# Optimization experiments

Measured on AMD Instinct MI355X. Metric: run time of the kernel, lower is better.

Reference implementation:

```python
import jax, jax.numpy as jnp
import numpy as np

DIM, NH, WS, SR, CTS = 256, 8, 8, 4, 2
HD = DIM // NH
SCALE = HD ** -0.5

def _linear(x, w, b=None):
    y = x @ w.T
    return y + b if b is not None else y

def _ln(x, g, b, eps=1e-5):
    m = jnp.mean(x, -1, keepdims=True)
    v = jnp.mean((x - m) ** 2, -1, keepdims=True)
    return (x - m) / jnp.sqrt(v + eps) * g + b

def _mlp(x, w1, b1, w2, b2):
    return _linear(jax.nn.gelu(_linear(x, w1, b1), approximate=False), w2, b2)

def _pos_emb_rank3(seq_len, w1, b1, w2):
    # PosEmbMLPSwinv1D with rank=3: coords on cube_root(seq) grid, normalized
    s = int(round(seq_len ** (1.0 / 3.0)))
    c = (jnp.arange(s, dtype=jnp.float32) - s // 2) / (s // 2)
    grid = jnp.stack(jnp.meshgrid(c, c, c, indexing='ij'))      # (3,s,s,s)
    tbl = grid.reshape(3, -1).T                                 # (s^3,3)
    return _linear(jax.nn.relu(_linear(tbl, w1, b1)), w2)[None]  # (1,s^3,dim)

def _rel_bias_3d(ws, w1, b1, w2, n_global):
    # PosEmbMLPSwinv3D: CPB-MLP bias over 3D relative coords, 16*sigmoid, zero-pad for carrier tokens
    r = jnp.arange(-(ws - 1), ws, dtype=jnp.float32)
    tbl = jnp.stack(jnp.meshgrid(r, r, r, indexing='ij'), axis=-1) / (ws - 1)
    tbl = tbl * 8.0
    tbl = jnp.sign(tbl) * jnp.log2(jnp.abs(tbl) + 1.0) / np.log2(8.0)
    table = _linear(jax.nn.relu(_linear(tbl.reshape(-1, 3), w1, b1)), w2)  # ((2ws-1)^3, NH)
    coords = jnp.stack(jnp.meshgrid(jnp.arange(ws), jnp.arange(ws), jnp.arange(ws), indexing='ij'))
    cf = coords.reshape(3, -1)
    rel = (cf[:, :, None] - cf[:, None, :]).transpose(1, 2, 0) + (ws - 1)  # (P,P,3)
    idx = rel[..., 0] * (2 * ws - 1) ** 2 + rel[..., 1] * (2 * ws - 1) + rel[..., 2]
    P = ws ** 3
    bias = table[idx.reshape(-1)].reshape(P, P, NH).transpose(2, 0, 1)
    bias = 16.0 * jax.nn.sigmoid(bias)
    return jnp.pad(bias, ((0, 0), (n_global, 0), (n_global, 0)))[None]  # (1,NH,P+g,P+g)

def _win_attn(x, qkv_w, qkv_b, proj_w, proj_b, bias):
    B, N, C = x.shape
    qkv = _linear(x, qkv_w, qkv_b).reshape(B, N, 3, NH, HD).transpose(2, 0, 3, 1, 4)
    q, k, v = qkv[0], qkv[1], qkv[2]
    attn = jax.nn.softmax(jnp.einsum('bhnd,bhmd->bhnm', q, k) * SCALE + bias, axis=-1)
    out = jnp.einsum('bhnm,bhmd->bhnd', attn, v).transpose(0, 2, 1, 3).reshape(B, N, C)
    return _linear(out, proj_w, proj_b)

def _ct_dewindow(ct, W, H, D, ws):
    bs, _, N = ct.shape
    c = ct.reshape(bs, W // ws, H // ws, D // ws, ws, ws, ws, N)
    c = c.transpose(0, 7, 1, 3, 5, 2, 4, 6).reshape(bs, N, W * H * D)
    return c.transpose(0, 2, 1)

def _ct_window(ct, W, H, D, ws):
    bs, _, N = ct.shape
    c = ct.reshape(bs, H // ws, ws, W // ws, ws, D // ws, ws, N)
    return c.transpose(0, 1, 3, 5, 2, 4, 6, 7)

def setup_inputs() -> dict:
    key = jax.random.key(0)
    ks = jax.random.split(key, 48)
    B0 = 1
    nw = SR ** 3
    def w(k, *s):
        return jax.random.normal(k, s, jnp.float32) * 0.02
    def b(k, *s):
        return jax.random.normal(k, s, jnp.float32) * 0.01
    d4 = 4 * DIM
    return {
        'x': jax.random.normal(ks[0], (B0 * nw, WS ** 3, DIM), jnp.float32),
        'ct': jax.random.normal(ks[1], (B0, (CTS * SR) ** 3, DIM), jnp.float32),
        'pe_w1': w(ks[2], 512, 3), 'pe_b1': b(ks[3], 512), 'pe_w2': w(ks[4], DIM, 512),
        'hpe_w1': w(ks[5], 512, 3), 'hpe_b1': b(ks[6], 512), 'hpe_w2': w(ks[7], DIM, 512),
        'hat_n1_g': jnp.ones((DIM,), jnp.float32), 'hat_n1_b': jnp.zeros((DIM,), jnp.float32),
        'hat_qkv_w': w(ks[8], 3 * DIM, DIM), 'hat_qkv_b': b(ks[9], 3 * DIM),
        'hat_proj_w': w(ks[10], DIM, DIM), 'hat_proj_b': b(ks[11], DIM),
        'hat_cpb_w1': w(ks[12], 512, 3), 'hat_cpb_b1': b(ks[13], 512), 'hat_cpb_w2': w(ks[14], NH, 512),
        'hat_n2_g': jnp.ones((DIM,), jnp.float32), 'hat_n2_b': jnp.zeros((DIM,), jnp.float32),
        'hat_fc1_w': w(ks[15], d4, DIM), 'hat_fc1_b': b(ks[16], d4),
        'hat_fc2_w': w(ks[17], DIM, d4), 'hat_fc2_b': b(ks[18], DIM),
        'n1_g': jnp.ones((DIM,), jnp.float32), 'n1_b': jnp.zeros((DIM,), jnp.float32),
        'qkv_w': w(ks[19], 3 * DIM, DIM), 'qkv_b': b(ks[20], 3 * DIM),
        'proj_w': w(ks[21], DIM, DIM), 'proj_b': b(ks[22], DIM),
        'cpb_w1': w(ks[23], 512, 3), 'cpb_b1': b(ks[24], 512), 'cpb_w2': w(ks[25], NH, 512),
        'n2_g': jnp.ones((DIM,), jnp.float32), 'n2_b': jnp.zeros((DIM,), jnp.float32),
        'fc1_w': w(ks[26], d4, DIM), 'fc1_b': b(ks[27], d4),
        'fc2_w': w(ks[28], DIM, d4), 'fc2_b': b(ks[29], DIM),
    }

def reference(x, ct, pe_w1, pe_b1, pe_w2, hpe_w1, hpe_b1, hpe_w2,
              hat_n1_g, hat_n1_b, hat_qkv_w, hat_qkv_b, hat_proj_w, hat_proj_b,
              hat_cpb_w1, hat_cpb_b1, hat_cpb_w2, hat_n2_g, hat_n2_b,
              hat_fc1_w, hat_fc1_b, hat_fc2_w, hat_fc2_b,
              n1_g, n1_b, qkv_w, qkv_b, proj_w, proj_b,
              cpb_w1, cpb_b1, cpb_w2, n2_g, n2_b, fc1_w, fc1_b, fc2_w, fc2_b):
    Bg, Ng, Hg = ct.shape
    G = CTS * SR  # carrier-token global cube side
    x = x + _pos_emb_rank3(x.shape[1], pe_w1, pe_b1, pe_w2)
    # carrier-token global attention (hierarchical path)
    ct = _ct_dewindow(ct, G, G, G, CTS)
    ct = ct + _pos_emb_rank3(ct.shape[1], hpe_w1, hpe_b1, hpe_w2)
    hat_bias = _rel_bias_3d(G, hat_cpb_w1, hat_cpb_b1, hat_cpb_w2, 0)
    ct = ct + _win_attn(_ln(ct, hat_n1_g, hat_n1_b), hat_qkv_w, hat_qkv_b, hat_proj_w, hat_proj_b, hat_bias)
    ct = ct + _mlp(_ln(ct, hat_n2_g, hat_n2_b), hat_fc1_w, hat_fc1_b, hat_fc2_w, hat_fc2_b)
    ct_w = _ct_window(ct, G, G, G, CTS).reshape(x.shape[0], -1, Hg)
    # windowed attention over [carrier tokens ; window tokens]
    x = jnp.concatenate([ct_w, x], axis=1)
    bias = _rel_bias_3d(WS, cpb_w1, cpb_b1, cpb_w2, CTS ** 3)
    x = x + _win_attn(_ln(x, n1_g, n1_b), qkv_w, qkv_b, proj_w, proj_b, bias)
    x = x + _mlp(_ln(x, n2_g, n2_b), fc1_w, fc1_b, fc2_w, fc2_b)
    split = x.shape[1] - WS ** 3
    ctr, x = x[:, :split], x[:, split:]
    return x, ctr.reshape(Bg, Ng, Hg)
```

## Files before the change

### kernel.cpp

```cpp
#include <hip/hip_runtime.h>
#include <hip/hip_bf16.h>
#include <math.h>

typedef __hip_bfloat16 bf16;

#define SCALE_QK 0.17677669529663687f

__device__ __forceinline__ float b2f(bf16 v){ return __bfloat162float(v); }
__device__ __forceinline__ bf16  f2b(float v){ return __float2bfloat16(v); }
__device__ __forceinline__ short bfs(float x){ bf16 b = f2b(x); short s; __builtin_memcpy(&s, &b, 2); return s; }

struct __align__(16) bf16x8 { bf16 v[8]; };
struct __align__(8)  bf16x4 { bf16 v[4]; };

typedef __attribute__((ext_vector_type(8))) short sh8;
typedef __attribute__((ext_vector_type(4))) short sh4;
typedef __attribute__((ext_vector_type(4))) float f4;

#if defined(__has_builtin)
#if __has_builtin(__builtin_amdgcn_mfma_f32_16x16x16bf16_1k)
#define HAS_MFMA16 1
#else
#define HAS_MFMA16 0
#endif
#else
#define HAS_MFMA16 0
#endif

#if defined(__has_builtin)
#if __has_builtin(__builtin_amdgcn_exp2f)
#define EXP2(x) __builtin_amdgcn_exp2f(x)
#else
#define EXP2(x) exp2f(x)
#endif
#else
#define EXP2(x) exp2f(x)
#endif

__device__ __forceinline__ void gl16(const bf16* g, short* l) {
    __builtin_amdgcn_global_load_lds((const __attribute__((address_space(1))) void*)g,
                                     (__attribute__((address_space(3))) void*)l, 16, 0, 0);
}

__global__ __launch_bounds__(256) void wcvt10_k(const float* s0, const float* s1, const float* s2, const float* s3,
                                                const float* s4, const float* s5, const float* s6, const float* s7,
                                                const float* s8, const float* s9,
                                                bf16* d0, bf16* d1, bf16* d2, bf16* d3, bf16* d4,
                                                bf16* d5, bf16* d6, bf16* d7, bf16* d8, bf16* d9) {
    const int sizes[10] = {196608, 65536, 262144, 262144, 196608, 65536, 262144, 262144, 131072, 131072};
    int which = blockIdx.y;
    const float* s; bf16* d;
    switch (which) {
        case 0: s = s0; d = d0; break;  case 1: s = s1; d = d1; break;
        case 2: s = s2; d = d2; break;  case 3: s = s3; d = d3; break;
        case 4: s = s4; d = d4; break;  case 5: s = s5; d = d5; break;
        case 6: s = s6; d = d6; break;  case 7: s = s7; d = d7; break;
        case 8: s = s8; d = d8; break;  default: s = s9; d = d9; break;
    }
    int i = blockIdx.x * 256 + threadIdx.x;
    if (i < sizes[which]) d[i] = f2b(s[i]);
}

__global__ __launch_bounds__(256) void hidbuild_k(const float* __restrict__ w1a, const float* __restrict__ b1a,
                                                  const float* __restrict__ w1b, const float* __restrict__ b1b,
                                                  bf16* __restrict__ hidA, bf16* __restrict__ hidB) {
    const float* w1 = blockIdx.y ? w1b : w1a;
    const float* b1 = blockIdx.y ? b1b : b1a;
    bf16* hid       = blockIdx.y ? hidB : hidA;
    int t = blockIdx.x, tid = threadIdx.x;
    int i = t >> 6, j = (t >> 3) & 7, k = t & 7;
    float c0 = (i - 4) * 0.25f, c1 = (j - 4) * 0.25f, c2 = (k - 4) * 0.25f;
    #pragma unroll
    for (int rep = 0; rep < 2; rep++) {
        int jj = tid + rep * 256;
        float h = c0 * w1[jj*3+0] + c1 * w1[jj*3+1] + c2 * w1[jj*3+2] + b1[jj];
        hid[(size_t)t * 512 + jj] = f2b(fmaxf(h, 0.f));
    }
}

__device__ __forceinline__ float cpb_coord(int idx) {
    float v = (idx - 7) * (8.0f / 7.0f);
    return copysignf(log2f(fabsf(v) + 1.0f) * (1.0f / 3.0f), v);
}
__global__ __launch_bounds__(512) void cpbtab_k(const float* __restrict__ w1a, const float* __restrict__ b1a,
                                                const float* __restrict__ w2a, float* __restrict__ taba,
                                                const float* __restrict__ w1b, const float* __restrict__ b1b,
                                                const float* __restrict__ w2b, float* __restrict__ tabb) {
    const float* w1 = blockIdx.y ? w1b : w1a;
    const float* b1 = blockIdx.y ? b1b : b1a;
    const float* w2 = blockIdx.y ? w2b : w2a;
    float* tab      = blockIdx.y ? tabb : taba;
    int t = blockIdx.x, tid = threadIdx.x;
    __shared__ float hid[512];
    int i = t / 225, r = t - i * 225, j = r / 15, k = r - j * 15;
    float x0 = cpb_coord(i), x1 = cpb_coord(j), x2 = cpb_coord(k);
    float h = x0 * w1[tid*3+0] + x1 * w1[tid*3+1] + x2 * w1[tid*3+2] + b1[tid];
    hid[tid] = fmaxf(h, 0.f);
    __syncthreads();
    int h8 = tid >> 6, lane = tid & 63;
    float p = 0.f;
    for (int jj = lane; jj < 512; jj += 64) p += hid[jj] * w2[h8*512 + jj];
    for (int off = 32; off; off >>= 1) p += __shfl_down(p, off);
    if (lane == 0) tab[t * 8 + h8] = p;
}

__global__ __launch_bounds__(256) void biasbuild_k(const float* __restrict__ taba, float* __restrict__ biasQa,
                                                   const float* __restrict__ tabb, float* __restrict__ biasQb) {
    const float* tab = blockIdx.y ? tabb : taba;
    float* biasQ     = blockIdx.y ? biasQb : biasQa;
    int idx = blockIdx.x * 256 + threadIdx.x;
    int h = idx >> 18, rem = idx & 262143;
    int q = rem >> 9, k = rem & 511;
    int qx = q >> 6, qy = (q >> 3) & 7, qz = q & 7;
    int kx = k >> 6, ky = (k >> 3) & 7, kz = k & 7;
    int tidx = ((qx - kx + 7) * 15 + (qy - ky + 7)) * 15 + (qz - kz + 7);
    float v = tab[tidx * 8 + h];
    float b = 16.f / (1.f + __expf(-v));
    biasQ[idx] = (b - 24.0f) * 1.4426950408889634f;
}

__global__ __launch_bounds__(256) void ct0ln_k(const float* __restrict__ ct_in,
                                               const float* __restrict__ hpe,
                                               const float* __restrict__ g,
                                               const float* __restrict__ b,
                                               float* __restrict__ ct0,
                                               bf16* __restrict__ lnout) {
    int u = blockIdx.x, c = threadIdx.x;
    int a = u >> 7, cc = (u >> 5) & 3, e = (u >> 4) & 1, bb = (u >> 2) & 3, d = (u >> 1) & 1, f = u & 1;
    int t = a * 128 + bb * 32 + cc * 8 + d * 4 + e * 2 + f;
    float x = ct_in[(size_t)t * 256 + c] + hpe[(size_t)u * 256 + c];
    ct0[(size_t)u * 256 + c] = x;
    float s = x, s2 = x * x;
    for (int off = 32; off; off >>= 1) { s += __shfl_down(s, off); s2 += __shfl_down(s2, off); }
    __shared__ float red[8];
    int wid = c >> 6, lane = c & 63;
    if (lane == 0) { red[wid] = s; red[wid + 4] = s2; }
    __syncthreads();
    if (c == 0) { red[0] = red[0] + red[1] + red[2] + red[3]; red[4] = red[4] + red[5] + red[6] + red[7]; }
    __syncthreads();
    float mean = red[0] * (1.f / 256.f);
    float var  = fmaxf(red[4] * (1.f / 256.f) - mean * mean, 0.f);
    float rstd = rsqrtf(var + 1e-5f);
    lnout[(size_t)u * 256 + c] = f2b((x - mean) * rstd * g[c] + b[c]);
}

__global__ __launch_bounds__(256) void ln_k(const float* __restrict__ in,
                                            const float* __restrict__ g,
                                            const float* __restrict__ b,
                                            bf16* __restrict__ out) {
    int row = blockIdx.x, c = threadIdx.x;
    float x = in[(size_t)row * 256 + c];
    float s = x, s2 = x * x;
    for (int off = 32; off; off >>= 1) { s += __shfl_down(s, off); s2 += __shfl_down(s2, off); }
    __shared__ float red[8];
    int wid = c >> 6, lane = c & 63;
    if (lane == 0) { red[wid] = s; red[wid + 4] = s2; }
    __syncthreads();
    if (c == 0) { red[0] = red[0] + red[1] + red[2] + red[3]; red[4] = red[4] + red[5] + red[6] + red[7]; }
    __syncthreads();
    float mean = red[0] * (1.f / 256.f);
    float var  = fmaxf(red[4] * (1.f / 256.f) - mean * mean, 0.f);
    float rstd = rsqrtf(var + 1e-5f);
    out[(size_t)row * 256 + c] = f2b((x - mean) * rstd * g[c] + b[c]);
}

template <int MODE>
__global__ __launch_bounds__(256) void gemm_k(const bf16* __restrict__ A,
                                              const bf16* __restrict__ W,
                                              const float* __restrict__ bias,
                                              int M, int N, int K,
                                              float* __restrict__ res,
                                              bf16* __restrict__ outb) {
    __shared__ short As[128 * 32];
    __shared__ short Ws[128 * 32];
    int m0 = blockIdx.y * 128, n0 = blockIdx.x * 128;
    int tid = threadIdx.x;
    int lane = tid & 63, wave = tid >> 6;
    int quad = lane >> 4, m16 = lane & 15;
    int wm = (wave & 1) * 64, wn = (wave >> 1) * 64;
    int arow = tid >> 2, acol = (tid & 3) * 8;

    const bf16* Ab = A + (size_t)(m0 + arow) * K + acol;
    const bf16* A2 = Ab + (size_t)64 * K;
    const bf16* Wb = W + (size_t)(n0 + arow) * K + acol;
    const bf16* W2 = Wb + (size_t)64 * K;
    short* dA0 = &As[tid * 8];
    short* dA1 = &As[2048 + tid * 8];
    short* dW0 = &Ws[tid * 8];
    short* dW1 = &Ws[2048 + tid * 8];

    f4 acc[4][4];
    #pragma unroll
    for (int i = 0; i < 4; i++)
        #pragma unroll
        for (int j = 0; j < 4; j++) acc[i][j] = (f4){0.f, 0.f, 0.f, 0.f};

    for (int k0 = 0; k0 < K; k0 += 32) {
        __syncthreads();
        gl16(Ab + k0, dA0);
        gl16(A2 + k0, dA1);
        gl16(Wb + k0, dW0);
        gl16(W2 + k0, dW1);
        __syncthreads();
        sh8 af[4], bf[4];
        #pragma unroll
        for (int mi = 0; mi < 4; mi++)
            af[mi] = *reinterpret_cast<const sh8*>(&As[(wm + mi * 16 + m16) * 32 + quad * 8]);
        #pragma unroll
        for (int ni = 0; ni < 4; ni++)
            bf[ni] = *reinterpret_cast<const sh8*>(&Ws[(wn + ni * 16 + m16) * 32 + quad * 8]);
        #pragma unroll
        for (int mi = 0; mi < 4; mi++)
            #pragma unroll
            for (int ni = 0; ni < 4; ni++)
                acc[mi][ni] = __builtin_amdgcn_mfma_f32_16x16x32_bf16(af[mi], bf[ni], acc[mi][ni], 0, 0, 0);
    }
    (void)M;

    #pragma unroll
    for (int mi = 0; mi < 4; mi++) {
        #pragma unroll
        for (int r = 0; r < 4; r++) {
            int gm = m0 + wm + mi * 16 + quad * 4 + r;
            #pragma unroll
            for (int ni = 0; ni < 4; ni++) {
                int gn = n0 + wn + ni * 16 + m16;
                float v = acc[mi][ni][r];
                if constexpr (MODE != 3) v += bias[gn];
                if constexpr (MODE == 2)      res[(size_t)gm * N + gn] += v;
                else if constexpr (MODE == 3) res[(size_t)gm * N + gn] = v;
                else if constexpr (MODE == 1) outb[(size_t)gm * N + gn] = f2b(0.5f * v * (1.0f + erff(v * 0.70710678118654752f)));
                else                          outb[(size_t)gm * N + gn] = f2b(v);
            }
        }
    }
}

__global__ __launch_bounds__(512) void gemmln_k(const bf16* __restrict__ A,
                                                const bf16* __restrict__ W,
                                                const float* __restrict__ bias,
                                                float* __restrict__ xcat,
                                                const float* __restrict__ g,
                                                const float* __restrict__ b,
                                                bf16* __restrict__ outb) {
    __shared__ short As[128 * 32];
    __shared__ short Ws[256 * 32];
    __shared__ float redS[128 * 4];
    __shared__ float redQ[128 * 4];
    __shared__ float stat[128 * 2];
    int m0 = blockIdx.x * 128;
    int tid = threadIdx.x;
    int lane = tid & 63, wave = tid >> 6;
    int quad = lane >> 4, m16 = lane & 15;
    int wm = (wave >> 2) * 64, wn = (wave & 3) * 64;
    int arow = tid >> 2, acol = (tid & 3) * 8;

    const bf16* Ab = A + (size_t)(m0 + (arow & 127)) * 256 + acol;
    const bf16* Wb = W + (size_t)arow * 256 + acol;
    const bf16* W2 = Wb + (size_t)128 * 256;
    short* dA0 = &As[(tid & 511) * 8 < 4096 ? tid * 8 : 0];

    f4 acc[4][4];
    #pragma unroll
    for (int i = 0; i < 4; i++)
        #pragma unroll
        for (int j = 0; j < 4; j++) acc[i][j] = (f4){0.f, 0.f, 0.f, 0.f};

    for (int k0 = 0; k0 < 256; k0 += 32) {
        __syncthreads();
        gl16(Ab + k0, &As[tid * 8]);
        gl16(Wb + k0, &Ws[tid * 8]);
        gl16(W2 + k0, &Ws[4096 + tid * 8]);
        __syncthreads();
        sh8 af[4], bf[4];
        #pragma unroll
        for (int mi = 0; mi < 4; mi++)
            af[mi] = *reinterpret_cast<const sh8*>(&As[(wm + mi * 16 + m16) * 32 + quad * 8]);
        #pragma unroll
        for (int ni = 0; ni < 4; ni++)
            bf[ni] = *reinterpret_cast<const sh8*>(&Ws[(wn + ni * 16 + m16) * 32 + quad * 8]);
        #pragma unroll
        for (int mi = 0; mi < 4; mi++)
            #pragma unroll
            for (int ni = 0; ni < 4; ni++)
                acc[mi][ni] = __builtin_amdgcn_mfma_f32_16x16x32_bf16(af[mi], bf[ni], acc[mi][ni], 0, 0, 0);
    }
    (void)dA0;

    #pragma unroll
    for (int mi = 0; mi < 4; mi++) {
        #pragma unroll
        for (int r = 0; r < 4; r++) {
            int lr = wm + mi * 16 + quad * 4 + r;
            int gm = m0 + lr;
            float ps = 0.f, pq = 0.f;
            #pragma unroll
            for (int ni = 0; ni < 4; ni++) {
                int gc = wn + ni * 16 + m16;
                float v = acc[mi][ni][r] + bias[gc] + xcat[(size_t)gm * 256 + gc];
                acc[mi][ni][r] = v;
                ps += v; pq += v * v;
            }
            ps += __shfl_xor(ps, 1); pq += __shfl_xor(pq, 1);
            ps += __shfl_xor(ps, 2); pq += __shfl_xor(pq, 2);
            ps += __shfl_xor(ps, 4); pq += __shfl_xor(pq, 4);
            ps += __shfl_xor(ps, 8); pq += __shfl_xor(pq, 8);
            if (m16 == 0) { redS[lr * 4 + (wave & 3)] = ps; redQ[lr * 4 + (wave & 3)] = pq; }
        }
    }
    __syncthreads();
    if (tid < 128) {
        float s = redS[tid * 4] + redS[tid * 4 + 1] + redS[tid * 4 + 2] + redS[tid * 4 + 3];
        float q = redQ[tid * 4] + redQ[tid * 4 + 1] + redQ[tid * 4 + 2] + redQ[tid * 4 + 3];
        float mean = s * (1.f / 256.f);
        float var  = fmaxf(q * (1.f / 256.f) - mean * mean, 0.f);
        stat[tid * 2]     = mean;
        stat[tid * 2 + 1] = rsqrtf(var + 1e-5f);
    }
    __syncthreads();
    #pragma unroll
    for (int mi = 0; mi < 4; mi++) {
        #pragma unroll
        for (int r = 0; r < 4; r++) {
            int lr = wm + mi * 16 + quad * 4 + r;
            int gm = m0 + lr;
            float mean = stat[lr * 2], rstd = stat[lr * 2 + 1];
            #pragma unroll
            for (int ni = 0; ni < 4; ni++) {
                int gc = wn + ni * 16 + m16;
                float v = acc[mi][ni][r];
                xcat[(size_t)gm * 256 + gc] = v;
                outb[(size_t)gm * 256 + gc] = f2b((v - mean) * rstd * g[gc] + b[gc]);
            }
        }
    }
}

__global__ __launch_bounds__(256) void gemmsplit_k(const bf16* __restrict__ A,
                                                   const bf16* __restrict__ W,
                                                   const float* __restrict__ bias,
                                                   int K,
                                                   const float* __restrict__ res,
                                                   float* __restrict__ out) {
    __shared__ short As[128 * 32];
    __shared__ short Ws[128 * 32];
    int m0 = blockIdx.y * 128, n0 = blockIdx.x * 128;
    int tid = threadIdx.x;
    int lane = tid & 63, wave = tid >> 6;
    int quad = lane >> 4, m16 = lane & 15;
    int wm = (wave & 1) * 64, wn = (wave >> 1) * 64;
    int arow = tid >> 2, acol = (tid & 3) * 8;

    const bf16* Ab = A + (size_t)(m0 + arow) * K + acol;
    const bf16* A2 = Ab + (size_t)64 * K;
    const bf16* Wb = W + (size_t)(n0 + arow) * K + acol;
    const bf16* W2 = Wb + (size_t)64 * K;

    f4 acc[4][4];
    #pragma unroll
    for (int i = 0; i < 4; i++)
        #pragma unroll
        for (int j = 0; j < 4; j++) acc[i][j] = (f4){0.f, 0.f, 0.f, 0.f};

    for (int k0 = 0; k0 < K; k0 += 32) {
        __syncthreads();
        gl16(Ab + k0, &As[tid * 8]);
        gl16(A2 + k0, &As[2048 + tid * 8]);
        gl16(Wb + k0, &Ws[tid * 8]);
        gl16(W2 + k0, &Ws[2048 + tid * 8]);
        __syncthreads();
        sh8 af[4], bf[4];
        #pragma unroll
        for (int mi = 0; mi < 4; mi++)
            af[mi] = *reinterpret_cast<const sh8*>(&As[(wm + mi * 16 + m16) * 32 + quad * 8]);
        #pragma unroll
        for (int ni = 0; ni < 4; ni++)
            bf[ni] = *reinterpret_cast<const sh8*>(&Ws[(wn + ni * 16 + m16) * 32 + quad * 8]);
        #pragma unroll
        for (int mi = 0; mi < 4; mi++)
            #pragma unroll
            for (int ni = 0; ni < 4; ni++)
                acc[mi][ni] = __builtin_amdgcn_mfma_f32_16x16x32_bf16(af[mi], bf[ni], acc[mi][ni], 0, 0, 0);
    }

    #pragma unroll
    for (int mi = 0; mi < 4; mi++) {
        #pragma unroll
        for (int r = 0; r < 4; r++) {
            int gm = m0 + wm + mi * 16 + quad * 4 + r;
            int w = gm / 520, p = gm - w * 520;
            size_t drow = (p >= 8) ? (size_t)(w * 512 + p - 8) : (size_t)(32768 + w * 8 + p);
            #pragma unroll
            for (int ni = 0; ni < 4; ni++) {
                int gn = n0 + wn + ni * 16 + m16;
                float v = acc[mi][ni][r] + bias[gn] + res[(size_t)gm * 256 + gn];
                out[drow * 256 + gn] = v;
            }
        }
    }
}

#define VSTR 548
#define SC2   0.25503575360579045f
#define CNB  (-34.62468098133512f)
#define NEGB (-1.0e30f)
__global__ __launch_bounds__(512) void flash_k(const bf16* __restrict__ qkv,
                                               const float* __restrict__ biasQ,
                                               bf16* __restrict__ out,
                                               int N, int glob) {
    int wh = blockIdx.x, w = wh >> 3, h = wh & 7;
    int qs = blockIdx.y;
    int tid = threadIdx.x;
    int lane = tid & 63, wave = tid >> 6;
    int quad = lane >> 4, qcol = lane & 15;
    const int NT32 = (N + 31) & ~31;

    __shared__ __align__(16) char smem[32 * VSTR * 2];
    bf16* Vt = reinterpret_cast<bf16*>(smem);
#if !HAS_MFMA16
    __shared__ float Ps[8][16 * 17];
#endif

    for (int i = tid; i < NT32 * 4; i += 512) {
        int tok = i >> 2, seg = i & 3;
        if (tok < N) {
            const bf16* vp = qkv + ((size_t)(w * N + tok)) * 768 + 512 + h * 32 + seg * 8;
            bf16x8 vv = *reinterpret_cast<const bf16x8*>(vp);
            #pragma unroll
            for (int e = 0; e < 8; e++) Vt[(seg * 8 + e) * VSTR + tok] = vv.v[e];
        } else {
            bf16 z = f2b(0.f);
            #pragma unroll
            for (int e = 0; e < 8; e++) Vt[(seg * 8 + e) * VSTR + tok] = z;
        }
    }
    __syncthreads();

    const bf16* qbase = qkv + ((size_t)w * N) * 768 + h * 32;
    const bf16* kbase = qbase + 256;
    int nqt = (N + 15) >> 4, nkt = NT32 >> 5;
    int nfull = nqt >> 1;

    if (qs < 2) {
        int u = wave + 8 * qs;
        if (u < nfull) {
            int qA = u * 32 + qcol;
            int qB = qA + 16;
            sh8 qfA = *reinterpret_cast<const sh8*>(qbase + (size_t)qA * 768 + quad * 8);
            sh8 qfB = *reinterpret_cast<const sh8*>(qbase + (size_t)qB * 768 + quad * 8);
            f4 O0A = {0.f,0.f,0.f,0.f}, O1A = {0.f,0.f,0.f,0.f};
            f4 O0B = {0.f,0.f,0.f,0.f}, O1B = {0.f,0.f,0.f,0.f};
            float lA = 0.f, lB = 0.f;
            bool vA = (qA >= glob);
            bool vB = (qB >= glob);
            const float* browA = biasQ + (((size_t)h << 9) + (size_t)(vA ? (qA - glob) : 0)) * 512 - glob;
            const float* browB = biasQ + (((size_t)h << 9) + (size_t)(vB ? (qB - glob) : 0)) * 512 - glob;

            sh8 kf0, kf1;
            {
                int k0 = qcol, k1 = 16 + qcol;
                kf0 = *reinterpret_cast<const sh8*>(kbase + (size_t)((k0 < N) ? k0 : (N - 1)) * 768 + quad * 8);
                kf1 = *reinterpret_cast<const sh8*>(kbase + (size_t)((k1 < N) ? k1 : (N - 1)) * 768 + quad * 8);
            }

            for (int kt = 0; kt < nkt; kt++) {
                int bt = kt * 32;
                sh8 c0 = kf0, c1 = kf1;
                if (kt + 1 < nkt) {
                    int n0 = bt + 32 + qcol, n1 = bt + 48 + qcol;
                    kf0 = *reinterpret_cast<const sh8*>(kbase + (size_t)((n0 < N) ? n0 : (N - 1)) * 768 + quad * 8);
                    kf1 = *reinterpret_cast<const sh8*>(kbase + (size_t)((n1 < N) ? n1 : (N - 1)) * 768 + quad * 8);
                }
                f4 z = {0.f, 0.f, 0.f, 0.f};
                f4 s0A = __builtin_amdgcn_mfma_f32_16x16x32_bf16(c0, qfA, z, 0, 0, 0);
                f4 s1A = __builtin_amdgcn_mfma_f32_16x16x32_bf16(c1, qfA, z, 0, 0, 0);
                f4 s0B = __builtin_amdgcn_mfma_f32_16x16x32_bf16(c0, qfB, z, 0, 0, 0);
                f4 s1B = __builtin_amdgcn_mfma_f32_16x16x32_bf16(c1, qfB, z, 0, 0, 0);

                int tg0 = bt + quad * 4, tg1 = bt + 16 + quad * 4;
                bool val0 = tg0 < N, val1 = tg1 < N;
                f4 bb0A, bb1A, bb0B, bb1B;
                if (!val0)                    bb0A = (f4){NEGB, NEGB, NEGB, NEGB};
                else if (vA && tg0 >= glob)   bb0A = *reinterpret_cast<const f4*>(browA + tg0);
                else                          bb0A = (f4){CNB, CNB, CNB, CNB};
                if (!val1)                    bb1A = (f4){NEGB, NEGB, NEGB, NEGB};
                else if (vA && tg1 >= glob)   bb1A = *reinterpret_cast<const f4*>(browA + tg1);
                else                          bb1A = (f4){CNB, CNB, CNB, CNB};
                if (!val0)                    bb0B = (f4){NEGB, NEGB, NEGB, NEGB};
                else if (vB && tg0 >= glob)   bb0B = *reinterpret_cast<const f4*>(browB + tg0);
                else                          bb0B = (f4){CNB, CNB, CNB, CNB};
                if (!val1)                    bb1B = (f4){NEGB, NEGB, NEGB, NEGB};
                else if (vB && tg1 >= glob)   bb1B = *reinterpret_cast<const f4*>(browB + tg1);
                else                          bb1B = (f4){CNB, CNB, CNB, CNB};

                float pA[8], pB[8];
                #pragma unroll
                for (int r = 0; r < 4; r++) {
                    pA[r]     = EXP2(fmaf(s0A[r], SC2, bb0A[r]));
                    pA[4 + r] = EXP2(fmaf(s1A[r], SC2, bb1A[r]));
                    pB[r]     = EXP2(fmaf(s0B[r], SC2, bb0B[r]));
                    pB[4 + r] = EXP2(fmaf(s1B[r], SC2, bb1B[r]));
                }
                #pragma unroll
                for (int r = 0; r < 8; r++) { lA += pA[r]; lB += pB[r]; }

#if HAS_MFMA16
                sh4 v00 = *reinterpret_cast<const sh4*>(&Vt[qcol * VSTR + bt + quad * 4]);
                sh4 v10 = *reinterpret_cast<const sh4*>(&Vt[qcol * VSTR + bt + 16 + quad * 4]);
                sh4 v01 = *reinterpret_cast<const sh4*>(&Vt[(qcol + 16) * VSTR + bt + quad * 4]);
                sh4 v11 = *reinterpret_cast<const sh4*>(&Vt[(qcol + 16) * VSTR + bt + 16 + quad * 4]);
                sh4 pf0A, pf1A, pf0B, pf1B;
                #pragma unroll
                for (int r = 0; r < 4; r++) {
                    pf0A[r] = bfs(pA[r]); pf1A[r] = bfs(pA[4 + r]);
                    pf0B[r] = bfs(pB[r]); pf1B[r] = bfs(pB[4 + r]);
                }
                O0A = __builtin_amdgcn_mfma_f32_16x16x16bf16_1k(v00, pf0A, O0A, 0, 0, 0);
                O0A = __builtin_amdgcn_mfma_f32_16x16x16bf16_1k(v10, pf1A, O0A, 0, 0, 0);
                O1A = __builtin_amdgcn_mfma_f32_16x16x16bf16_1k(v01, pf0A, O1A, 0, 0, 0);
                O1A = __builtin_amdgcn_mfma_f32_16x16x16bf16_1k(v11, pf1A, O1A, 0, 0, 0);
                O0B = __builtin_amdgcn_mfma_f32_16x16x16bf16_1k(v00, pf0B, O0B, 0, 0, 0);
                O0B = __builtin_amdgcn_mfma_f32_16x16x16bf16_1k(v10, pf1B, O0B, 0, 0, 0);
                O1B = __builtin_amdgcn_mfma_f32_16x16x16bf16_1k(v01, pf0B, O1B, 0, 0, 0);
                O1B = __builtin_amdgcn_mfma_f32_16x16x16bf16_1k(v11, pf1B, O1B, 0, 0, 0);
#else
                for (int t = 0; t < 2; t++) {
                    const float* ph = t ? pB : pA;
                    for (int half = 0; half < 2; half++) {
                        #pragma unroll
                        for (int r = 0; r < 4; r++) Ps[wave][(quad * 4 + r) * 17 + qcol] = ph[half * 4 + r];
                        __builtin_amdgcn_wave_barrier();
                        sh8 pbig, va, vb;
                        #pragma unroll
                        for (int j = 0; j < 8; j++) {
                            int tl = quad * 8 + j;
                            float pv = (quad < 2) ? Ps[wave][tl * 17 + qcol] : 0.f;
                            pbig[j] = bfs(pv);
                            bf16 a0 = (quad < 2) ? Vt[qcol * VSTR + bt + half * 16 + tl] : f2b(0.f);
                            bf16 a1 = (quad < 2) ? Vt[(qcol + 16) * VSTR + bt + half * 16 + tl] : f2b(0.f);
                            short t0, t1;
                            __builtin_memcpy(&t0, &a0, 2); __builtin_memcpy(&t1, &a1, 2);
                            va[j] = t0; vb[j] = t1;
                        }
                        if (t == 0) {
                            O0A = __builtin_amdgcn_mfma_f32_16x16x32_bf16(va, pbig, O0A, 0, 0, 0);
                            O1A = __builtin_amdgcn_mfma_f32_16x16x32_bf16(vb, pbig, O1A, 0, 0, 0);
                        } else {
                            O0B = __builtin_amdgcn_mfma_f32_16x16x32_bf16(va, pbig, O0B, 0, 0, 0);
                            O1B = __builtin_amdgcn_mfma_f32_16x16x32_bf16(vb, pbig, O1B, 0, 0, 0);
                        }
                        __builtin_amdgcn_wave_barrier();
                    }
                }
#endif
            }

            lA += __shfl_xor(lA, 16); lA += __shfl_xor(lA, 32);
            lB += __shfl_xor(lB, 16); lB += __shfl_xor(lB, 32);
            float rlA = 1.f / lA, rlB = 1.f / lB;
            {
                bf16x4 o0, o1;
                #pragma unroll
                for (int r = 0; r < 4; r++) { o0.v[r] = f2b(O0A[r] * rlA); o1.v[r] = f2b(O1A[r] * rlA); }
                bf16* op = out + ((size_t)(w * N + qA)) * 256 + h * 32 + quad * 4;
                *reinterpret_cast<bf16x4*>(op)      = o0;
                *reinterpret_cast<bf16x4*>(op + 16) = o1;
            }
            {
                bf16x4 o0, o1;
                #pragma unroll
                for (int r = 0; r < 4; r++) { o0.v[r] = f2b(O0B[r] * rlB); o1.v[r] = f2b(O1B[r] * rlB); }
                bf16* op = out + ((size_t)(w * N + qB)) * 256 + h * 32 + quad * 4;
                *reinterpret_cast<bf16x4*>(op)      = o0;
                *reinterpret_cast<bf16x4*>(op + 16) = o1;
            }
        }
    } else {
        int rt = nqt - 1;
        int qA = rt * 16 + qcol;
        int qrA = (qA < N) ? qA : (N - 1);
        sh8 qfA = *reinterpret_cast<const sh8*>(qbase + (size_t)qrA * 768 + quad * 8);
        f4 O0 = {0.f,0.f,0.f,0.f}, O1 = {0.f,0.f,0.f,0.f};
        float l = 0.f;
        bool vA = (qA >= glob) && (qA < N);
        const float* browA = biasQ + (((size_t)h << 9) + (size_t)(vA ? (qA - glob) : 0)) * 512 - glob;

        for (int kt = wave; kt < nkt; kt += 8) {
            int bt = kt * 32;
            int k0 = bt + qcol, k1 = bt + 16 + qcol;
            sh8 c0 = *reinterpret_cast<const sh8*>(kbase + (size_t)((k0 < N) ? k0 : (N - 1)) * 768 + quad * 8);
            sh8 c1 = *reinterpret_cast<const sh8*>(kbase + (size_t)((k1 < N) ? k1 : (N - 1)) * 768 + quad * 8);
            f4 z = {0.f, 0.f, 0.f, 0.f};
            f4 s0 = __builtin_amdgcn_mfma_f32_16x16x32_bf16(c0, qfA, z, 0, 0, 0);
            f4 s1 = __builtin_amdgcn_mfma_f32_16x16x32_bf16(c1, qfA, z, 0, 0, 0);

            int tg0 = bt + quad * 4, tg1 = bt + 16 + quad * 4;
            bool val0 = tg0 < N, val1 = tg1 < N;
            f4 bb0, bb1;
            if (!val0)                    bb0 = (f4){NEGB, NEGB, NEGB, NEGB};
            else if (vA && tg0 >= glob)   bb0 = *reinterpret_cast<const f4*>(browA + tg0);
            else                          bb0 = (f4){CNB, CNB, CNB, CNB};
            if (!val1)                    bb1 = (f4){NEGB, NEGB, NEGB, NEGB};
            else if (vA && tg1 >= glob)   bb1 = *reinterpret_cast<const f4*>(browA + tg1);
            else                          bb1 = (f4){CNB, CNB, CNB, CNB};

            float p[8];
            #pragma unroll
            for (int r = 0; r < 4; r++) {
                p[r]     = EXP2(fmaf(s0[r], SC2, bb0[r]));
                p[4 + r] = EXP2(fmaf(s1[r], SC2, bb1[r]));
            }
            #pragma unroll
            for (int r = 0; r < 8; r++) l += p[r];

#if HAS_MFMA16
            sh4 v00 = *reinterpret_cast<const sh4*>(&Vt[qcol * VSTR + bt + quad * 4]);
            sh4 v10 = *reinterpret_cast<const sh4*>(&Vt[qcol * VSTR + bt + 16 + quad * 4]);
            sh4 v01 = *reinterpret_cast<const sh4*>(&Vt[(qcol + 16) * VSTR + bt + quad * 4]);
            sh4 v11 = *reinterpret_cast<const sh4*>(&Vt[(qcol + 16) * VSTR + bt + 16 + quad * 4]);
            sh4 pf0, pf1;
            #pragma unroll
            for (int r = 0; r < 4; r++) { pf0[r] = bfs(p[r]); pf1[r] = bfs(p[4 + r]); }
            O0 = __builtin_amdgcn_mfma_f32_16x16x16bf16_1k(v00, pf0, O0, 0, 0, 0);
            O0 = __builtin_amdgcn_mfma_f32_16x16x16bf16_1k(v10, pf1, O0, 0, 0, 0);
            O1 = __builtin_amdgcn_mfma_f32_16x16x16bf16_1k(v01, pf0, O1, 0, 0, 0);
            O1 = __builtin_amdgcn_mfma_f32_16x16x16bf16_1k(v11, pf1, O1, 0, 0, 0);
#else
            for (int half = 0; half < 2; half++) {
                #pragma unroll
                for (int r = 0; r < 4; r++) Ps[wave][(quad * 4 + r) * 17 + qcol] = p[half * 4 + r];
                __builtin_amdgcn_wave_barrier();
                sh8 pbig, va, vb;
                #pragma unroll
                for (int j = 0; j < 8; j++) {
                    int tl = quad * 8 + j;
                    float pv = (quad < 2) ? Ps[wave][tl * 17 + qcol] : 0.f;
                    pbig[j] = bfs(pv);
                    bf16 a0 = (quad < 2) ? Vt[qcol * VSTR + bt + half * 16 + tl] : f2b(0.f);
                    bf16 a1 = (quad < 2) ? Vt[(qcol + 16) * VSTR + bt + half * 16 + tl] : f2b(0.f);
                    short t0, t1;
                    __builtin_memcpy(&t0, &a0, 2); __builtin_memcpy(&t1, &a1, 2);
                    va[j] = t0; vb[j] = t1;
                }
                O0 = __builtin_amdgcn_mfma_f32_16x16x32_bf16(va, pbig, O0, 0, 0, 0);
                O1 = __builtin_amdgcn_mfma_f32_16x16x32_bf16(vb, pbig, O1, 0, 0, 0);
                __builtin_amdgcn_wave_barrier();
            }
#endif
        }

        __syncthreads();
        float (*red)[64][9] = reinterpret_cast<float (*)[64][9]>(smem);
        #pragma unroll
        for (int r = 0; r < 4; r++) { red[wave][lane][r] = O0[r]; red[wave][lane][4 + r] = O1[r]; }
        red[wave][lane][8] = l;
        __syncthreads();

        if (wave == 0) {
            f4 O0s = {0.f,0.f,0.f,0.f}, O1s = {0.f,0.f,0.f,0.f};
            float ls = 0.f;
            for (int v = 0; v < 8; v++) {
                #pragma unroll
                for (int r = 0; r < 4; r++) { O0s[r] += red[v][lane][r]; O1s[r] += red[v][lane][4 + r]; }
                ls += red[v][lane][8];
            }
            ls += __shfl_xor(ls, 16); ls += __shfl_xor(ls, 32);
            float rl = 1.f / ls;
            if (qA < N) {
                bf16x4 o0, o1;
                #pragma unroll
                for (int r = 0; r < 4; r++) { o0.v[r] = f2b(O0s[r] * rl); o1.v[r] = f2b(O1s[r] * rl); }
                bf16* op = out + ((size_t)(w * N + qA)) * 256 + h * 32 + quad * 4;
                *reinterpret_cast<bf16x4*>(op)      = o0;
                *reinterpret_cast<bf16x4*>(op + 16) = o1;
            }
        }
    }
}

__global__ __launch_bounds__(256) void xcatln_k(const float* __restrict__ x_in,
                                                const float* __restrict__ pe,
                                                const float* __restrict__ ct2,
                                                const float* __restrict__ g,
                                                const float* __restrict__ b,
                                                float* __restrict__ xcat,
                                                bf16* __restrict__ xln) {
    int row = blockIdx.x, w = row / 520, p = row - w * 520, c = threadIdx.x;
    float v;
    if (p < 8) {
        int P = w >> 4, Q = (w >> 2) & 3, R = w & 3;
        int S = p >> 2, T = (p >> 1) & 1, U = p & 1;
        int t = P * 128 + S * 64 + Q * 16 + T * 8 + R * 2 + U;
        v = ct2[(size_t)t * 256 + c];
    } else {
        int t = p - 8;
        v = x_in[((size_t)w * 512 + t) * 256 + c] + pe[(size_t)t * 256 + c];
    }
    xcat[(size_t)row * 256 + c] = v;
    float s = v, s2 = v * v;
    for (int off = 32; off; off >>= 1) { s += __shfl_down(s, off); s2 += __shfl_down(s2, off); }
    __shared__ float red[8];
    int wid = c >> 6, lane = c & 63;
    if (lane == 0) { red[wid] = s; red[wid + 4] = s2; }
    __syncthreads();
    if (c == 0) { red[0] = red[0] + red[1] + red[2] + red[3]; red[4] = red[4] + red[5] + red[6] + red[7]; }
    __syncthreads();
    float mean = red[0] * (1.f / 256.f);
    float var  = fmaxf(red[4] * (1.f / 256.f) - mean * mean, 0.f);
    float rstd = rsqrtf(var + 1e-5f);
    xln[(size_t)row * 256 + c] = f2b((v - mean) * rstd * g[c] + b[c]);
}

__global__ __launch_bounds__(256) void xcatbuild_k(const float* __restrict__ x_in,
                                                   const float* __restrict__ pe,
                                                   const float* __restrict__ ct2,
                                                   float* __restrict__ xcat) {
    int row = blockIdx.x, w = row / 520, p = row - w * 520, c = threadIdx.x;
    float v;
    if (p < 8) {
        int P = w >> 4, Q = (w >> 2) & 3, R = w & 3;
        int S = p >> 2, T = (p >> 1) & 1, U = p & 1;
        int t = P * 128 + S * 64 + Q * 16 + T * 8 + R * 2 + U;
        v = ct2[(size_t)t * 256 + c];
    } else {
        int t = p - 8;
        v = x_in[((size_t)w * 512 + t) * 256 + c] + pe[(size_t)t * 256 + c];
    }
    xcat[(size_t)row * 256 + c] = v;
}

__global__ __launch_bounds__(256) void outbuild_k(const float* __restrict__ xcat,
                                                  float* __restrict__ out) {
    int row = blockIdx.x, w = row / 520, p = row - w * 520, c = threadIdx.x;
    float v = xcat[(size_t)row * 256 + c];
    if (p >= 8) out[((size_t)(w * 512) + (p - 8)) * 256 + c] = v;
    else        out[(size_t)8388608 + ((size_t)(w * 8) + p) * 256 + c] = v;
}

extern "C" void kernel_launch(void* const* d_in, const int* in_sizes, int n_in,
                              void* d_out, int out_size, void* d_ws, size_t ws_size,
                              hipStream_t stream) {
    const float* x          = (const float*)d_in[0];
    const float* ct         = (const float*)d_in[1];
    const float* pe_w1      = (const float*)d_in[2];
    const float* pe_b1      = (const float*)d_in[3];
    const float* pe_w2      = (const float*)d_in[4];
    const float* hpe_w1     = (const float*)d_in[5];
    const float* hpe_b1     = (const float*)d_in[6];
    const float* hpe_w2     = (const float*)d_in[7];
    const float* hat_n1_g   = (const float*)d_in[8];
    const float* hat_n1_b   = (const float*)d_in[9];
    const float* hat_qkv_w  = (const float*)d_in[10];
    const float* hat_qkv_b  = (const float*)d_in[11];
    const float* hat_proj_w = (const float*)d_in[12];
    const float* hat_proj_b = (const float*)d_in[13];
    const float* hat_cpb_w1 = (const float*)d_in[14];
    const float* hat_cpb_b1 = (const float*)d_in[15];
    const float* hat_cpb_w2 = (const float*)d_in[16];
    const float* hat_n2_g   = (const float*)d_in[17];
    const float* hat_n2_b   = (const float*)d_in[18];
    const float* hat_fc1_w  = (const float*)d_in[19];
    const float* hat_fc1_b  = (const float*)d_in[20];
    const float* hat_fc2_w  = (const float*)d_in[21];
    const float* hat_fc2_b  = (const float*)d_in[22];
    const float* n1_g       = (const float*)d_in[23];
    const float* n1_b       = (const float*)d_in[24];
    const float* qkv_w      = (const float*)d_in[25];
    const float* qkv_b      = (const float*)d_in[26];
    const float* proj_w     = (const float*)d_in[27];
    const float* proj_b     = (const float*)d_in[28];
    const float* cpb_w1     = (const float*)d_in[29];
    const float* cpb_b1     = (const float*)d_in[30];
    const float* cpb_w2     = (const float*)d_in[31];
    const float* n2_g       = (const float*)d_in[32];
    const float* n2_b       = (const float*)d_in[33];
    const float* fc1_w      = (const float*)d_in[34];
    const float* fc1_b      = (const float*)d_in[35];
    const float* fc2_w      = (const float*)d_in[36];
    const float* fc2_b      = (const float*)d_in[37];
    (void)in_sizes; (void)n_in; (void)out_size;

    char* base = (char*)d_ws;
    size_t off = 0;
    auto alloc = [&](size_t bytes) -> void* {
        void* p = base + off;
        off += (bytes + 255) & ~(size_t)255;
        return p;
    };
    float* pe        = (float*)alloc(512 * 256 * 4);
    float* hpe       = (float*)alloc(512 * 256 * 4);
    float* tab_hat   = (float*)alloc(3375 * 8 * 4);
    float* tab2      = (float*)alloc(3375 * 8 * 4);
    float* biasQ2    = (float*)alloc((size_t)8 * 512 * 512 * 4);
    float* ct0       = (float*)alloc(512 * 256 * 4);
    bf16* wb_hqkv  = (bf16*)alloc(768 * 256 * 2);
    bf16* wb_hproj = (bf16*)alloc(256 * 256 * 2);
    bf16* wb_hfc1  = (bf16*)alloc(1024 * 256 * 2);
    bf16* wb_hfc2  = (bf16*)alloc(256 * 1024 * 2);
    bf16* wb_qkv   = (bf16*)alloc(768 * 256 * 2);
    bf16* wb_proj  = (bf16*)alloc(256 * 256 * 2);
    bf16* wb_fc1   = (bf16*)alloc(1024 * 256 * 2);
    bf16* wb_fc2   = (bf16*)alloc(256 * 1024 * 2);
    bf16* wb_pew2  = (bf16*)alloc(256 * 512 * 2);
    bf16* wb_hpew2 = (bf16*)alloc(256 * 512 * 2);
    size_t zstart = off;
    bf16*  hidA      = (bf16*)alloc(512 * 512 * 2);
    bf16*  hidB      = (bf16*)alloc(512 * 512 * 2);
    off = zstart;
    float* biasQ_hat = (float*)alloc((size_t)8 * 512 * 512 * 4);
    bf16*  hct_ln    = (bf16*)alloc(512 * 256 * 2);
    bf16*  hqkv      = (bf16*)alloc(512 * 768 * 2);
    bf16*  hat_attn  = (bf16*)alloc(512 * 256 * 2);
    bf16*  hat_hid   = (bf16*)alloc(512 * 1024 * 2);
    off = zstart;
    float* xcat      = (float*)alloc((size_t)64 * 520 * 256 * 4);
    const int S     = (ws_size >= (size_t)150 * 1024 * 1024) ? 1 : 4;
    const int rows  = 33280 / S;
    const int wins  = 64 / S;
    bf16*  xln_b     = (bf16*)alloc((size_t)rows * 256 * 2);
    char*  region_qa = (char*)alloc((size_t)rows * 1024 * 2);
    bf16*  qkv_b_    = (bf16*)region_qa;
    bf16*  attn_b    = (bf16*)(region_qa + (size_t)rows * 768 * 2);
    bf16*  hidden    = (bf16*)region_qa;

    wcvt10_k<<<dim3(1024, 10), 256, 0, stream>>>(hat_qkv_w, hat_proj_w, hat_fc1_w, hat_fc2_w,
                                                 qkv_w, proj_w, fc1_w, fc2_w, pe_w2, hpe_w2,
                                                 wb_hqkv, wb_hproj, wb_hfc1, wb_hfc2,
                                                 wb_qkv, wb_proj, wb_fc1, wb_fc2, wb_pew2, wb_hpew2);

    hidbuild_k<<<dim3(512, 2), 256, 0, stream>>>(pe_w1, pe_b1, hpe_w1, hpe_b1, hidA, hidB);
    gemm_k<3><<<dim3(2, 4), 256, 0, stream>>>(hidA, wb_pew2,  nullptr, 512, 256, 512, pe,  nullptr);
    gemm_k<3><<<dim3(2, 4), 256, 0, stream>>>(hidB, wb_hpew2, nullptr, 512, 256, 512, hpe, nullptr);

    cpbtab_k<<<dim3(3375, 2), 512, 0, stream>>>(hat_cpb_w1, hat_cpb_b1, hat_cpb_w2, tab_hat,
                                                cpb_w1, cpb_b1, cpb_w2, tab2);
    biasbuild_k<<<dim3(8192, 2), 256, 0, stream>>>(tab_hat, biasQ_hat, tab2, biasQ2);

    ct0ln_k<<<512, 256, 0, stream>>>(ct, hpe, hat_n1_g, hat_n1_b, ct0, hct_ln);
    gemm_k<0><<<dim3(6, 4), 256, 0, stream>>>(hct_ln, wb_hqkv, hat_qkv_b, 512, 768, 256, nullptr, hqkv);
    flash_k<<<dim3(8, 2), 512, 0, stream>>>(hqkv, biasQ_hat, hat_attn, 512, 0);
    gemmln_k<<<4, 512, 0, stream>>>(hat_attn, wb_hproj, hat_proj_b, ct0, hat_n2_g, hat_n2_b, hct_ln);
    gemm_k<1><<<dim3(8, 4), 256, 0, stream>>>(hct_ln, wb_hfc1, hat_fc1_b, 512, 1024, 256, nullptr, hat_hid);
    gemm_k<2><<<dim3(2, 4), 256, 0, stream>>>(hat_hid, wb_hfc2, hat_fc2_b, 512, 256, 1024, ct0, nullptr);

    if (S == 1) {
        xcatln_k<<<33280, 256, 0, stream>>>(x, pe, ct0, n1_g, n1_b, xcat, xln_b);
        gemm_k<0><<<dim3(6, 260), 256, 0, stream>>>(xln_b, wb_qkv, qkv_b, 33280, 768, 256, nullptr, qkv_b_);
        flash_k<<<dim3(512, 3), 512, 0, stream>>>(qkv_b_, biasQ2, attn_b, 520, 8);
        gemmln_k<<<260, 512, 0, stream>>>(attn_b, wb_proj, proj_b, xcat, n2_g, n2_b, xln_b);
        gemm_k<1><<<dim3(8, 260), 256, 0, stream>>>(xln_b, wb_fc1, fc1_b, 33280, 1024, 256, nullptr, hidden);
        gemmsplit_k<<<dim3(2, 260), 256, 0, stream>>>(hidden, wb_fc2, fc2_b, 1024, xcat, (float*)d_out);
    } else {
        xcatbuild_k<<<33280, 256, 0, stream>>>(x, pe, ct0, xcat);
        for (int s = 0; s < S; s++) {
            float* xc = xcat + (size_t)s * rows * 256;
            ln_k<<<rows, 256, 0, stream>>>(xc, n1_g, n1_b, xln_b);
            gemm_k<0><<<dim3(6, rows / 128), 256, 0, stream>>>(xln_b, wb_qkv, qkv_b, rows, 768, 256, nullptr, qkv_b_);
            flash_k<<<dim3(wins * 8, 3), 512, 0, stream>>>(qkv_b_, biasQ2, attn_b, 520, 8);
            gemm_k<2><<<dim3(2, rows / 128), 256, 0, stream>>>(attn_b, wb_proj, proj_b, rows, 256, 256, xc, nullptr);
        }
        for (int s = 0; s < S; s++) {
            float* xc = xcat + (size_t)s * rows * 256;
            ln_k<<<rows, 256, 0, stream>>>(xc, n2_g, n2_b, xln_b);
            gemm_k<1><<<dim3(8, rows / 128), 256, 0, stream>>>(xln_b, wb_fc1, fc1_b, rows, 1024, 256, nullptr, hidden);
            gemm_k<2><<<dim3(2, rows / 128), 256, 0, stream>>>(hidden, wb_fc2, fc2_b, rows, 256, 1024, xc, nullptr);
        }
        outbuild_k<<<33280, 256, 0, stream>>>(xcat, (float*)d_out);
    }
}
```

Measured before the change: 599.8 us.

## Double-buffer LDS tiles in GEMM kernels and prefetch attention bias

Converts the three MFMA GEMM kernels to double-buffered shared memory: the next K-tile's global loads are issued before the current tile's MFMAs, which removes one barrier per iteration. In the flash attention kernel, the relative-position bias loads for the next key tile are prefetched together with the K fragments. The bias selection is factored into a helper. The cost is twice the LDS per block for the GEMMs, which can lower occupancy, plus extra registers held for the prefetched bias.

```diff
diff --git a/kernel.cpp b/kernel.cpp
--- a/kernel.cpp
+++ b/kernel.cpp
@@ -171,8 +171,8 @@
                                               int M, int N, int K,
                                               float* __restrict__ res,
                                               bf16* __restrict__ outb) {
-    __shared__ short As[128 * 32];
-    __shared__ short Ws[128 * 32];
+    __shared__ short As[2][128 * 32];
+    __shared__ short Ws[2][128 * 32];
     int m0 = blockIdx.y * 128, n0 = blockIdx.x * 128;
     int tid = threadIdx.x;
     int lane = tid & 63, wave = tid >> 6;
@@ -184,10 +184,6 @@
     const bf16* A2 = Ab + (size_t)64 * K;
     const bf16* Wb = W + (size_t)(n0 + arow) * K + acol;
     const bf16* W2 = Wb + (size_t)64 * K;
-    short* dA0 = &As[tid * 8];
-    short* dA1 = &As[2048 + tid * 8];
-    short* dW0 = &Ws[tid * 8];
-    short* dW1 = &Ws[2048 + tid * 8];
 
     f4 acc[4][4];
     #pragma unroll
@@ -195,25 +191,35 @@
         #pragma unroll
         for (int j = 0; j < 4; j++) acc[i][j] = (f4){0.f, 0.f, 0.f, 0.f};
 
+    gl16(Ab, &As[0][tid * 8]);
+    gl16(A2, &As[0][2048 + tid * 8]);
+    gl16(Wb, &Ws[0][tid * 8]);
+    gl16(W2, &Ws[0][2048 + tid * 8]);
+    __syncthreads();
+
+    int cur = 0;
     for (int k0 = 0; k0 < K; k0 += 32) {
-        __syncthreads();
-        gl16(Ab + k0, dA0);
-        gl16(A2 + k0, dA1);
-        gl16(Wb + k0, dW0);
-        gl16(W2 + k0, dW1);
-        __syncthreads();
+        int nxt = cur ^ 1;
+        if (k0 + 32 < K) {
+            gl16(Ab + k0 + 32, &As[nxt][tid * 8]);
+            gl16(A2 + k0 + 32, &As[nxt][2048 + tid * 8]);
+            gl16(Wb + k0 + 32, &Ws[nxt][tid * 8]);
+            gl16(W2 + k0 + 32, &Ws[nxt][2048 + tid * 8]);
+        }
         sh8 af[4], bf[4];
         #pragma unroll
         for (int mi = 0; mi < 4; mi++)
-            af[mi] = *reinterpret_cast<const sh8*>(&As[(wm + mi * 16 + m16) * 32 + quad * 8]);
+            af[mi] = *reinterpret_cast<const sh8*>(&As[cur][(wm + mi * 16 + m16) * 32 + quad * 8]);
         #pragma unroll
         for (int ni = 0; ni < 4; ni++)
-            bf[ni] = *reinterpret_cast<const sh8*>(&Ws[(wn + ni * 16 + m16) * 32 + quad * 8]);
+            bf[ni] = *reinterpret_cast<const sh8*>(&Ws[cur][(wn + ni * 16 + m16) * 32 + quad * 8]);
         #pragma unroll
         for (int mi = 0; mi < 4; mi++)
             #pragma unroll
             for (int ni = 0; ni < 4; ni++)
                 acc[mi][ni] = __builtin_amdgcn_mfma_f32_16x16x32_bf16(af[mi], bf[ni], acc[mi][ni], 0, 0, 0);
+        __syncthreads();
+        cur = nxt;
     }
     (void)M;
 
@@ -243,8 +249,8 @@
                                                 const float* __restrict__ g,
                                                 const float* __restrict__ b,
                                                 bf16* __restrict__ outb) {
-    __shared__ short As[128 * 32];
-    __shared__ short Ws[256 * 32];
+    __shared__ short As[2][128 * 32];
+    __shared__ short Ws[2][256 * 32];
     __shared__ float redS[128 * 4];
     __shared__ float redQ[128 * 4];
     __shared__ float stat[128 * 2];
@@ -255,10 +261,9 @@
     int wm = (wave >> 2) * 64, wn = (wave & 3) * 64;
     int arow = tid >> 2, acol = (tid & 3) * 8;
 
-    const bf16* Ab = A + (size_t)(m0 + (arow & 127)) * 256 + acol;
+    const bf16* Ab = A + (size_t)(m0 + arow) * 256 + acol;
     const bf16* Wb = W + (size_t)arow * 256 + acol;
     const bf16* W2 = Wb + (size_t)128 * 256;
-    short* dA0 = &As[(tid & 511) * 8 < 4096 ? tid * 8 : 0];
 
     f4 acc[4][4];
     #pragma unroll
@@ -266,26 +271,34 @@
         #pragma unroll
         for (int j = 0; j < 4; j++) acc[i][j] = (f4){0.f, 0.f, 0.f, 0.f};
 
+    gl16(Ab, &As[0][tid * 8]);
+    gl16(Wb, &Ws[0][tid * 8]);
+    gl16(W2, &Ws[0][4096 + tid * 8]);
+    __syncthreads();
+
+    int cur = 0;
     for (int k0 = 0; k0 < 256; k0 += 32) {
-        __syncthreads();
-        gl16(Ab + k0, &As[tid * 8]);
-        gl16(Wb + k0, &Ws[tid * 8]);
-        gl16(W2 + k0, &Ws[4096 + tid * 8]);
-        __syncthreads();
+        int nxt = cur ^ 1;
+        if (k0 + 32 < 256) {
+            gl16(Ab + k0 + 32, &As[nxt][tid * 8]);
+            gl16(Wb + k0 + 32, &Ws[nxt][tid * 8]);
+            gl16(W2 + k0 + 32, &Ws[nxt][4096 + tid * 8]);
+        }
         sh8 af[4], bf[4];
         #pragma unroll
         for (int mi = 0; mi < 4; mi++)
-            af[mi] = *reinterpret_cast<const sh8*>(&As[(wm + mi * 16 + m16) * 32 + quad * 8]);
+            af[mi] = *reinterpret_cast<const sh8*>(&As[cur][(wm + mi * 16 + m16) * 32 + quad * 8]);
         #pragma unroll
         for (int ni = 0; ni < 4; ni++)
-            bf[ni] = *reinterpret_cast<const sh8*>(&Ws[(wn + ni * 16 + m16) * 32 + quad * 8]);
+            bf[ni] = *reinterpret_cast<const sh8*>(&Ws[cur][(wn + ni * 16 + m16) * 32 + quad * 8]);
         #pragma unroll
         for (int mi = 0; mi < 4; mi++)
             #pragma unroll
             for (int ni = 0; ni < 4; ni++)
                 acc[mi][ni] = __builtin_amdgcn_mfma_f32_16x16x32_bf16(af[mi], bf[ni], acc[mi][ni], 0, 0, 0);
-    }
-    (void)dA0;
+        __syncthreads();
+        cur = nxt;
+    }
 
     #pragma unroll
     for (int mi = 0; mi < 4; mi++) {
@@ -342,8 +355,8 @@
                                                    int K,
                                                    const float* __restrict__ res,
                                                    float* __restrict__ out) {
-    __shared__ short As[128 * 32];
-    __shared__ short Ws[128 * 32];
+    __shared__ short As[2][128 * 32];
+    __shared__ short Ws[2][128 * 32];
     int m0 = blockIdx.y * 128, n0 = blockIdx.x * 128;
     int tid = threadIdx.x;
     int lane = tid & 63, wave = tid >> 6;
@@ -362,25 +375,35 @@
         #pragma unroll
         for (int j = 0; j < 4; j++) acc[i][j] = (f4){0.f, 0.f, 0.f, 0.f};
 
+    gl16(Ab, &As[0][tid * 8]);
+    gl16(A2, &As[0][2048 + tid * 8]);
+    gl16(Wb, &Ws[0][tid * 8]);
+    gl16(W2, &Ws[0][2048 + tid * 8]);
+    __syncthreads();
+
+    int cur = 0;
     for (int k0 = 0; k0 < K; k0 += 32) {
-        __syncthreads();
-        gl16(Ab + k0, &As[tid * 8]);
-        gl16(A2 + k0, &As[2048 + tid * 8]);
-        gl16(Wb + k0, &Ws[tid * 8]);
-        gl16(W2 + k0, &Ws[2048 + tid * 8]);
-        __syncthreads();
+        int nxt = cur ^ 1;
+        if (k0 + 32 < K) {
+            gl16(Ab + k0 + 32, &As[nxt][tid * 8]);
+            gl16(A2 + k0 + 32, &As[nxt][2048 + tid * 8]);
+            gl16(Wb + k0 + 32, &Ws[nxt][tid * 8]);
+            gl16(W2 + k0 + 32, &Ws[nxt][2048 + tid * 8]);
+        }
         sh8 af[4], bf[4];
         #pragma unroll
         for (int mi = 0; mi < 4; mi++)
-            af[mi] = *reinterpret_cast<const sh8*>(&As[(wm + mi * 16 + m16) * 32 + quad * 8]);
+            af[mi] = *reinterpret_cast<const sh8*>(&As[cur][(wm + mi * 16 + m16) * 32 + quad * 8]);
         #pragma unroll
         for (int ni = 0; ni < 4; ni++)
-            bf[ni] = *reinterpret_cast<const sh8*>(&Ws[(wn + ni * 16 + m16) * 32 + quad * 8]);
+            bf[ni] = *reinterpret_cast<const sh8*>(&Ws[cur][(wn + ni * 16 + m16) * 32 + quad * 8]);
         #pragma unroll
         for (int mi = 0; mi < 4; mi++)
             #pragma unroll
             for (int ni = 0; ni < 4; ni++)
                 acc[mi][ni] = __builtin_amdgcn_mfma_f32_16x16x32_bf16(af[mi], bf[ni], acc[mi][ni], 0, 0, 0);
+        __syncthreads();
+        cur = nxt;
     }
 
     #pragma unroll
@@ -404,6 +427,11 @@
 #define SC2   0.25503575360579045f
 #define CNB  (-34.62468098133512f)
 #define NEGB (-1.0e30f)
+__device__ __forceinline__ f4 bias_ld(const float* brow, bool vq, int tg, int N, int glob) {
+    if (tg >= N) return (f4){NEGB, NEGB, NEGB, NEGB};
+    if (vq && tg >= glob) return *reinterpret_cast<const f4*>(brow + tg);
+    return (f4){CNB, CNB, CNB, CNB};
+}
 __global__ __launch_bounds__(512) void flash_k(const bf16* __restrict__ qkv,
                                                const float* __restrict__ biasQ,
                                                bf16* __restrict__ out,
@@ -457,41 +485,38 @@
             const float* browB = biasQ + (((size_t)h << 9) + (size_t)(vB ? (qB - glob) : 0)) * 512 - glob;
 
             sh8 kf0, kf1;
+            f4 nb0A, nb1A, nb0B, nb1B;
             {
                 int k0 = qcol, k1 = 16 + qcol;
                 kf0 = *reinterpret_cast<const sh8*>(kbase + (size_t)((k0 < N) ? k0 : (N - 1)) * 768 + quad * 8);
                 kf1 = *reinterpret_cast<const sh8*>(kbase + (size_t)((k1 < N) ? k1 : (N - 1)) * 768 + quad * 8);
+                int tg0 = quad * 4, tg1 = 16 + quad * 4;
+                nb0A = bias_ld(browA, vA, tg0, N, glob);
+                nb1A = bias_ld(browA, vA, tg1, N, glob);
+                nb0B = bias_ld(browB, vB, tg0, N, glob);
+                nb1B = bias_ld(browB, vB, tg1, N, glob);
             }
 
             for (int kt = 0; kt < nkt; kt++) {
                 int bt = kt * 32;
                 sh8 c0 = kf0, c1 = kf1;
+                f4 bb0A = nb0A, bb1A = nb1A, bb0B = nb0B, bb1B = nb1B;
                 if (kt + 1 < nkt) {
-                    int n0 = bt + 32 + qcol, n1 = bt + 48 + qcol;
+                    int btn = bt + 32;
+                    int n0 = btn + qcol, n1 = btn + 16 + qcol;
                     kf0 = *reinterpret_cast<const sh8*>(kbase + (size_t)((n0 < N) ? n0 : (N - 1)) * 768 + quad * 8);
                     kf1 = *reinterpret_cast<const sh8*>(kbase + (size_t)((n1 < N) ? n1 : (N - 1)) * 768 + quad * 8);
+                    int tg0n = btn + quad * 4, tg1n = btn + 16 + quad * 4;
+                    nb0A = bias_ld(browA, vA, tg0n, N, glob);
+                    nb1A = bias_ld(browA, vA, tg1n, N, glob);
+                    nb0B = bias_ld(browB, vB, tg0n, N, glob);
+                    nb1B = bias_ld(browB, vB, tg1n, N, glob);
                 }
                 f4 z = {0.f, 0.f, 0.f, 0.f};
                 f4 s0A = __builtin_amdgcn_mfma_f32_16x16x32_bf16(c0, qfA, z, 0, 0, 0);
                 f4 s1A = __builtin_amdgcn_mfma_f32_16x16x32_bf16(c1, qfA, z, 0, 0, 0);
                 f4 s0B = __builtin_amdgcn_mfma_f32_16x16x32_bf16(c0, qfB, z, 0, 0, 0);
                 f4 s1B = __builtin_amdgcn_mfma_f32_16x16x32_bf16(c1, qfB, z, 0, 0, 0);
-
-                int tg0 = bt + quad * 4, tg1 = bt + 16 + quad * 4;
-                bool val0 = tg0 < N, val1 = tg1 < N;
-                f4 bb0A, bb1A, bb0B, bb1B;
-                if (!val0)                    bb0A = (f4){NEGB, NEGB, NEGB, NEGB};
-                else if (vA && tg0 >= glob)   bb0A = *reinterpret_cast<const f4*>(browA + tg0);
-                else                          bb0A = (f4){CNB, CNB, CNB, CNB};
-                if (!val1)                    bb1A = (f4){NEGB, NEGB, NEGB, NEGB};
-                else if (vA && tg1 >= glob)   bb1A = *reinterpret_cast<const f4*>(browA + tg1);
-                else                          bb1A = (f4){CNB, CNB, CNB, CNB};
-                if (!val0)                    bb0B = (f4){NEGB, NEGB, NEGB, NEGB};
-                else if (vB && tg0 >= glob)   bb0B = *reinterpret_cast<const f4*>(browB + tg0);
-                else                          bb0B = (f4){CNB, CNB, CNB, CNB};
-                if (!val1)                    bb1B = (f4){NEGB, NEGB, NEGB, NEGB};
-                else if (vB && tg1 >= glob)   bb1B = *reinterpret_cast<const f4*>(browB + tg1);
-                else                          bb1B = (f4){CNB, CNB, CNB, CNB};
 
                 float pA[8], pB[8];
                 #pragma unroll
@@ -595,14 +620,8 @@
             f4 s1 = __builtin_amdgcn_mfma_f32_16x16x32_bf16(c1, qfA, z, 0, 0, 0);
 
             int tg0 = bt + quad * 4, tg1 = bt + 16 + quad * 4;
-            bool val0 = tg0 < N, val1 = tg1 < N;
-            f4 bb0, bb1;
-            if (!val0)                    bb0 = (f4){NEGB, NEGB, NEGB, NEGB};
-            else if (vA && tg0 >= glob)   bb0 = *reinterpret_cast<const f4*>(browA + tg0);
-            else                          bb0 = (f4){CNB, CNB, CNB, CNB};
-            if (!val1)                    bb1 = (f4){NEGB, NEGB, NEGB, NEGB};
-            else if (vA && tg1 >= glob)   bb1 = *reinterpret_cast<const f4*>(browA + tg1);
-            else                          bb1 = (f4){CNB, CNB, CNB, CNB};
+            f4 bb0 = bias_ld(browA, vA, tg0, N, glob);
+            f4 bb1 = bias_ld(browA, vA, tg1, N, glob);
 
             float p[8];
             #pragma unroll
```

After: 583.1 us. 2.8% less time.
